# Kernel tuning notes

Measured on AMD Instinct MI355X. Metric: run time of the kernel, lower is better.

## Reference

```python
import jax, jax.numpy as jnp
import numpy as np

N_CELL, N_GENE, D, E = 100000, 20000, 128, 1000000


def setup_inputs() -> dict:
    key = jax.random.key(0)
    ks = jax.random.split(key, 16)
    return {
        "cell_z": jax.random.normal(ks[0], (N_CELL, D), jnp.float32),
        "gene_z": jax.random.normal(ks[1], (N_GENE, D), jnp.float32),
        "W_gene": jax.random.normal(ks[2], (D, D), jnp.float32) / np.sqrt(D),
        "b_gene": jax.random.normal(ks[3], (D,), jnp.float32) * 0.01,
        "cell_scale": jax.random.normal(ks[4], (N_CELL,), jnp.float32),
        "cell_bias": jax.random.normal(ks[5], (N_CELL,), jnp.float32),
        "cell_std": jax.random.uniform(ks[6], (N_CELL,), jnp.float32, 0.1, 1.0),
        "gene_scale": jax.random.normal(ks[7], (N_GENE,), jnp.float32),
        "gene_bias": jax.random.normal(ks[8], (N_GENE,), jnp.float32),
        "gene_std": jax.random.uniform(ks[9], (N_GENE,), jnp.float32, 0.1, 1.0),
        "src_idx": jax.random.randint(ks[10], (E,), 0, N_CELL, jnp.int32),
        "dst_idx": jax.random.randint(ks[11], (E,), 0, N_GENE, jnp.int32),
        "cell_n_id": jax.random.randint(ks[12], (N_CELL,), 0, N_CELL, jnp.int32),
        "gene_n_id": jax.random.randint(ks[13], (N_GENE,), 0, N_GENE, jnp.int32),
    }


def reference(cell_z, gene_z, W_gene, b_gene,
              cell_scale, cell_bias, cell_std,
              gene_scale, gene_bias, gene_std,
              src_idx, dst_idx, cell_n_id, gene_n_id):
    # Relation projection: 'cell' -> Identity, 'gene' -> Linear + LeakyReLU.
    # Project per-node then gather (mathematically identical to the original
    # gather-then-project since projection is pointwise per node).
    gene_proj = jax.nn.leaky_relu(gene_z @ W_gene + b_gene)  # [N_GENE, D]
    u = cell_z[src_idx]            # [E, D] gather of src node embeddings
    v = gene_proj[dst_idx]         # [E, D] gather of projected dst embeddings

    # Per-edge scale/bias/std lookups via global node ids (n_id[edge_index]).
    sid = cell_n_id[src_idx]       # [E]
    did = gene_n_id[dst_idx]       # [E]
    s_sc, s_b, s_sd = cell_scale[sid], cell_bias[sid], cell_std[sid]
    d_sc, d_b, d_sd = gene_scale[did], gene_bias[did], gene_std[did]

    dot = jnp.sum(u * v, axis=-1)  # [E]
    loc = dot * s_sc * d_sc + s_b + d_b
    std = s_sd * d_sd
    return jnp.stack([loc, std])   # [2, E]
```

## Files before the change

kernel.cpp:

```cpp
#include <hip/hip_runtime.h>

#define N_CELL 100000
#define N_GENE 20000
#define DIM    128
#define N_EDGE 1000000

#define NS_STRIPE 20
#define NTILE     40
#define NBLK_SORT 977

#define NB_WCAST 8
#define NB_CTAB  391
#define NB_GTAB  79
#define NB_MISC  (NB_WCAST + NB_CTAB + NB_GTAB)

#define NB_PROJ  625
#define NB_HIST  977
#define NB_CAST  6250

typedef float f32x4 __attribute__((ext_vector_type(4)));

__device__ inline unsigned short f2bf(float f) {
    unsigned u = __float_as_uint(f);
    u += 0x7fffu + ((u >> 16) & 1u);
    return (unsigned short)(u >> 16);
}

__device__ inline void dot2(float& acc, unsigned a, unsigned b) {
    asm("v_dot2_f32_bf16 %0, %1, %2, %0" : "+v"(acc) : "v"(a), "v"(b));
}

__device__ inline int tile_of(int s, int d) {
    const int ss = (int)(((unsigned long long)s * 429497ULL) >> 31);
    const int ds = (d >= 10000) ? 1 : 0;
    return ds * NS_STRIPE + ss;
}

__device__ inline unsigned pack_sd(int s, int d) {
    return ((unsigned)s << 15) | (unsigned)d;
}

__device__ inline float lrelu(float v) { return v > 0.f ? v : 0.01f * v; }

__global__ __launch_bounds__(256) void misc_kernel(
    const float* __restrict__ W,
    ushort* __restrict__ Wbt,
    const int*   __restrict__ cell_n_id,
    const int*   __restrict__ gene_n_id,
    const float* __restrict__ cell_scale,
    const float* __restrict__ cell_bias,
    const float* __restrict__ cell_std,
    const float* __restrict__ gene_scale,
    const float* __restrict__ gene_bias,
    const float* __restrict__ gene_std,
    float4* __restrict__ cell_p4,
    float4* __restrict__ gene_p4)
{
    const int tid = threadIdx.x;
    int blk = blockIdx.x;

    if (blk < NB_WCAST) {
        const int t   = blk * 256 + tid;
        const int col = t >> 4;
        const int k8  = t & 15;
        unsigned short w[8];
        #pragma unroll
        for (int j = 0; j < 8; ++j)
            w[j] = f2bf(W[(k8 * 8 + j) * DIM + col]);
        uint4 o;
        o.x = (unsigned)w[0] | ((unsigned)w[1] << 16);
        o.y = (unsigned)w[2] | ((unsigned)w[3] << 16);
        o.z = (unsigned)w[4] | ((unsigned)w[5] << 16);
        o.w = (unsigned)w[6] | ((unsigned)w[7] << 16);
        ((uint4*)Wbt)[t] = o;
        return;
    }
    blk -= NB_WCAST;

    if (blk < NB_CTAB) {
        if (!cell_p4) return;
        const int c = blk * 256 + tid;
        if (c < N_CELL) {
            const int id = cell_n_id[c];
            cell_p4[c] = make_float4(cell_scale[id], cell_bias[id],
                                     cell_std[id], 0.f);
        }
        return;
    }
    blk -= NB_CTAB;

    if (!gene_p4) return;
    const int g = blk * 256 + tid;
    if (g < N_GENE) {
        const int id = gene_n_id[g];
        gene_p4[g] = make_float4(gene_scale[id], gene_bias[id],
                                 gene_std[id], 0.f);
    }
}

__global__ __launch_bounds__(256) void proj_kernel(
    const float* __restrict__ gene_z,
    const float* __restrict__ b,
    const ushort* __restrict__ Wbt,
    ushort* __restrict__ gene_projb)
{
    __shared__ ushort zb[32 * DIM];
    __shared__ uint4  wl[2048];

    const int tid = threadIdx.x;

    const uint4* wg = (const uint4*)Wbt;
    #pragma unroll
    for (int i = 0; i < 8; ++i) {
        const int u = i * 256 + tid;
        const int c = u >> 4, j = u & 15;
        wl[(c << 4) | (j ^ (c & 15))] = wg[u];
    }

    const int row0 = blockIdx.x * 32;
    const f32x4* Z4 = (const f32x4*)(gene_z + (long)row0 * DIM);
    #pragma unroll
    for (int i = 0; i < 4; ++i) {
        const int idx = i * 256 + tid;
        const f32x4 v = Z4[idx];
        ushort4 o;
        o.x = f2bf(v.x); o.y = f2bf(v.y); o.z = f2bf(v.z); o.w = f2bf(v.w);
        ((ushort4*)zb)[idx] = o;
    }
    __syncthreads();

    const int cg = tid & 31;
    const int rg = tid >> 5;

    const float4 bb = ((const float4*)b)[cg];
    float acc[4][4];
    #pragma unroll
    for (int r = 0; r < 4; ++r) {
        acc[r][0] = bb.x; acc[r][1] = bb.y; acc[r][2] = bb.z; acc[r][3] = bb.w;
    }

    const uint4* zr = (const uint4*)zb;
    #pragma unroll 4
    for (int k8 = 0; k8 < 16; ++k8) {
        uint4 z[4], w[4];
        #pragma unroll
        for (int r = 0; r < 4; ++r)
            z[r] = zr[(rg * 4 + r) * 16 + k8];
        #pragma unroll
        for (int c = 0; c < 4; ++c) {
            const int col = cg * 4 + c;
            w[c] = wl[(col << 4) | (k8 ^ (col & 15))];
        }
        #pragma unroll
        for (int r = 0; r < 4; ++r)
            #pragma unroll
            for (int c = 0; c < 4; ++c) {
                dot2(acc[r][c], z[r].x, w[c].x);
                dot2(acc[r][c], z[r].y, w[c].y);
                dot2(acc[r][c], z[r].z, w[c].z);
                dot2(acc[r][c], z[r].w, w[c].w);
            }
    }

    #pragma unroll
    for (int r = 0; r < 4; ++r) {
        ushort4 o;
        o.x = f2bf(lrelu(acc[r][0]));
        o.y = f2bf(lrelu(acc[r][1]));
        o.z = f2bf(lrelu(acc[r][2]));
        o.w = f2bf(lrelu(acc[r][3]));
        *(ushort4*)(gene_projb + (long)(row0 + rg * 4 + r) * DIM + cg * 4) = o;
    }
}

__global__ __launch_bounds__(256) void hist_kernel(
    const int* __restrict__ src_idx,
    const int* __restrict__ dst_idx,
    int* __restrict__ counts)
{
    __shared__ int lcnt[NTILE];
    const int tid = threadIdx.x;
    const int blk = blockIdx.x;
    if (tid < NTILE) lcnt[tid] = 0;
    __syncthreads();
    #pragma unroll
    for (int q = 0; q < 4; ++q) {
        const int e = blk * 1024 + q * 256 + tid;
        if (e < N_EDGE) {
            const int t = tile_of(src_idx[e], dst_idx[e]);
            atomicAdd(&lcnt[t], 1);
        }
    }
    __syncthreads();
    if (tid < NTILE) counts[tid * NBLK_SORT + blk] = lcnt[tid];
}

__global__ __launch_bounds__(256) void cast_kernel(
    const float* __restrict__ cell_z, ushort4* __restrict__ cell_zb4)
{
    const f32x4* in4 = (const f32x4*)cell_z;
    const int base = blockIdx.x * 512 + threadIdx.x;
    const f32x4 v0 = in4[base];
    const f32x4 v1 = in4[base + 256];
    ushort4 o0, o1;
    o0.x = f2bf(v0.x); o0.y = f2bf(v0.y); o0.z = f2bf(v0.z); o0.w = f2bf(v0.w);
    o1.x = f2bf(v1.x); o1.y = f2bf(v1.y); o1.z = f2bf(v1.z); o1.w = f2bf(v1.w);
    cell_zb4[base]       = o0;
    cell_zb4[base + 256] = o1;
}

__global__ __launch_bounds__(256) void scanA_kernel(
    int* __restrict__ counts, int* __restrict__ totals)
{
    __shared__ int sd[256];
    const int t   = blockIdx.x;
    const int tid = threadIdx.x;
    int carry = 0;
    for (int c = 0; c < 4; ++c) {
        const int idx = c * 256 + tid;
        const int val = (idx < NBLK_SORT) ? counts[t * NBLK_SORT + idx] : 0;
        sd[tid] = val;
        __syncthreads();
        #pragma unroll
        for (int off = 1; off < 256; off <<= 1) {
            const int tmp = (tid >= off) ? sd[tid - off] : 0;
            __syncthreads();
            sd[tid] += tmp;
            __syncthreads();
        }
        const int incl = sd[tid];
        const int ctot = sd[255];
        if (idx < NBLK_SORT) counts[t * NBLK_SORT + idx] = carry + incl - val;
        carry += ctot;
        __syncthreads();
    }
    if (tid == 0) totals[t] = carry;
}

__global__ __launch_bounds__(256) void scatter_kernel(
    const int* __restrict__ src_idx,
    const int* __restrict__ dst_idx,
    const int* __restrict__ counts,
    const int* __restrict__ totals,
    unsigned* __restrict__ sorted_p,
    int*      __restrict__ rank)
{
    __shared__ int lcnt[NTILE];
    __shared__ int sbase[NTILE];
    __shared__ int lbase[NTILE];
    const int tid = threadIdx.x;
    const int blk = blockIdx.x;
    if (tid < NTILE) lcnt[tid] = 0;
    __syncthreads();

    int ts[4], rs[4], ss[4], ds[4];
    #pragma unroll
    for (int c = 0; c < 4; ++c) {
        const int e = blk * 1024 + c * 256 + tid;
        if (e < N_EDGE) {
            ss[c] = src_idx[e];
            ds[c] = dst_idx[e];
            ts[c] = tile_of(ss[c], ds[c]);
            rs[c] = atomicAdd(&lcnt[ts[c]], 1);
        } else { ts[c] = -1; rs[c] = 0; ss[c] = 0; ds[c] = 0; }
    }
    __syncthreads();
    if (tid == 0) {
        int s = 0;
        for (int i = 0; i < NTILE; ++i) { sbase[i] = s; s += totals[i]; }
    }
    __syncthreads();
    if (tid < NTILE) lbase[tid] = sbase[tid] + counts[tid * NBLK_SORT + blk];
    __syncthreads();

    #pragma unroll
    for (int c = 0; c < 4; ++c) {
        const int e = blk * 1024 + c * 256 + tid;
        if (ts[c] >= 0) {
            const int pos = lbase[ts[c]] + rs[c];
            sorted_p[pos] = pack_sd(ss[c], ds[c]);
            rank[e] = pos;
        }
    }
}

__global__ __launch_bounds__(256) void edge_sorted_kernel(
    const ushort* __restrict__ cell_zb,
    const ushort* __restrict__ gene_projb,
    const unsigned* __restrict__ sorted_p,
    const float4* __restrict__ cell_p4,
    const float4* __restrict__ gene_p4,
    float2* __restrict__ res)
{
    const int wg  = blockIdx.x;
    const int xcd = wg & 7;
    const int sub = wg >> 3;
    const int q = 15625 / 8, r = 15625 % 8;
    const int swz = ((xcd < r) ? xcd * (q + 1) : r * (q + 1) + (xcd - r) * q) + sub;

    const int tid  = threadIdx.x;
    const int lane = tid & 15;
    const int grp  = swz * 16 + (tid >> 4);

    const uint4 p = ((const uint4*)sorted_p)[grp];
    const int s0 = (int)(p.x >> 15), d0 = (int)(p.x & 0x7fffu);
    const int s1 = (int)(p.y >> 15), d1 = (int)(p.y & 0x7fffu);
    const int s2 = (int)(p.z >> 15), d2 = (int)(p.z & 0x7fffu);
    const int s3 = (int)(p.w >> 15), d3 = (int)(p.w & 0x7fffu);

    uint4 a0 = ((const uint4*)(cell_zb    + (long)s0 * DIM))[lane];
    uint4 a1 = ((const uint4*)(cell_zb    + (long)s1 * DIM))[lane];
    uint4 a2 = ((const uint4*)(cell_zb    + (long)s2 * DIM))[lane];
    uint4 a3 = ((const uint4*)(cell_zb    + (long)s3 * DIM))[lane];
    uint4 v0 = ((const uint4*)(gene_projb + (long)d0 * DIM))[lane];
    uint4 v1 = ((const uint4*)(gene_projb + (long)d1 * DIM))[lane];
    uint4 v2 = ((const uint4*)(gene_projb + (long)d2 * DIM))[lane];
    uint4 v3 = ((const uint4*)(gene_projb + (long)d3 * DIM))[lane];

    float dot0 = 0.f, dot1 = 0.f, dot2v = 0.f, dot3 = 0.f;
    dot2(dot0, a0.x, v0.x); dot2(dot0, a0.y, v0.y);
    dot2(dot0, a0.z, v0.z); dot2(dot0, a0.w, v0.w);
    dot2(dot1, a1.x, v1.x); dot2(dot1, a1.y, v1.y);
    dot2(dot1, a1.z, v1.z); dot2(dot1, a1.w, v1.w);
    dot2(dot2v, a2.x, v2.x); dot2(dot2v, a2.y, v2.y);
    dot2(dot2v, a2.z, v2.z); dot2(dot2v, a2.w, v2.w);
    dot2(dot3, a3.x, v3.x); dot2(dot3, a3.y, v3.y);
    dot2(dot3, a3.z, v3.z); dot2(dot3, a3.w, v3.w);

    #define RED(d)                 \
        d += __shfl_xor(d, 1);     \
        d += __shfl_xor(d, 2);     \
        d += __shfl_xor(d, 4);     \
        d += __shfl_xor(d, 8);
    RED(dot0) RED(dot1) RED(dot2v) RED(dot3)
    #undef RED

    if (lane < 4) {
        const float dj = (lane & 2) ? ((lane & 1) ? dot3 : dot2v)
                                    : ((lane & 1) ? dot1 : dot0);
        const int sj   = (lane & 2) ? ((lane & 1) ? s3 : s2)
                                    : ((lane & 1) ? s1 : s0);
        const int djx  = (lane & 2) ? ((lane & 1) ? d3 : d2)
                                    : ((lane & 1) ? d1 : d0);
        const float4 cs = cell_p4[sj];
        const float4 gs = gene_p4[djx];
        res[grp * 4 + lane] =
            make_float2(dj * cs.x * gs.x + cs.y + gs.y, cs.z * gs.z);
    }
}

__global__ __launch_bounds__(256) void fixup_kernel(
    const int*    __restrict__ rank,
    const float2* __restrict__ res,
    float* __restrict__ out)
{
    const int e0 = (blockIdx.x * 256 + threadIdx.x) * 4;
    if (e0 >= N_EDGE) return;
    const int4 r4 = *(const int4*)(rank + e0);
    const float2 r0 = res[r4.x];
    const float2 r1 = res[r4.y];
    const float2 r2 = res[r4.z];
    const float2 r3 = res[r4.w];
    *(float4*)(out + e0)          = make_float4(r0.x, r1.x, r2.x, r3.x);
    *(float4*)(out + N_EDGE + e0) = make_float4(r0.y, r1.y, r2.y, r3.y);
}

template<bool TAB>
__global__ __launch_bounds__(256) void edge_kernel(
    const ushort* __restrict__ cell_zb,
    const ushort* __restrict__ gene_projb,
    const int*   __restrict__ src_idx,
    const int*   __restrict__ dst_idx,
    const int*   __restrict__ cell_n_id,
    const int*   __restrict__ gene_n_id,
    const float* __restrict__ cell_scale,
    const float* __restrict__ cell_bias,
    const float* __restrict__ cell_std,
    const float* __restrict__ gene_scale,
    const float* __restrict__ gene_bias,
    const float* __restrict__ gene_std,
    const float4* __restrict__ cell_p4,
    const float4* __restrict__ gene_p4,
    float* __restrict__ out)
{
    const int tid  = threadIdx.x;
    const int lane = tid & 15;
    const int grp  = blockIdx.x * 16 + (tid >> 4);
    const int e0   = grp * 4;

    const int4 s4 = ((const int4*)src_idx)[grp];
    const int4 d4 = ((const int4*)dst_idx)[grp];

    uint4 a0 = ((const uint4*)(cell_zb    + (long)s4.x * DIM))[lane];
    uint4 a1 = ((const uint4*)(cell_zb    + (long)s4.y * DIM))[lane];
    uint4 a2 = ((const uint4*)(cell_zb    + (long)s4.z * DIM))[lane];
    uint4 a3 = ((const uint4*)(cell_zb    + (long)s4.w * DIM))[lane];
    uint4 v0 = ((const uint4*)(gene_projb + (long)d4.x * DIM))[lane];
    uint4 v1 = ((const uint4*)(gene_projb + (long)d4.y * DIM))[lane];
    uint4 v2 = ((const uint4*)(gene_projb + (long)d4.z * DIM))[lane];
    uint4 v3 = ((const uint4*)(gene_projb + (long)d4.w * DIM))[lane];

    float dot0 = 0.f, dot1 = 0.f, dot2v = 0.f, dot3 = 0.f;
    dot2(dot0, a0.x, v0.x); dot2(dot0, a0.y, v0.y);
    dot2(dot0, a0.z, v0.z); dot2(dot0, a0.w, v0.w);
    dot2(dot1, a1.x, v1.x); dot2(dot1, a1.y, v1.y);
    dot2(dot1, a1.z, v1.z); dot2(dot1, a1.w, v1.w);
    dot2(dot2v, a2.x, v2.x); dot2(dot2v, a2.y, v2.y);
    dot2(dot2v, a2.z, v2.z); dot2(dot2v, a2.w, v2.w);
    dot2(dot3, a3.x, v3.x); dot2(dot3, a3.y, v3.y);
    dot2(dot3, a3.z, v3.z); dot2(dot3, a3.w, v3.w);

    #define RED(d)                 \
        d += __shfl_xor(d, 1);     \
        d += __shfl_xor(d, 2);     \
        d += __shfl_xor(d, 4);     \
        d += __shfl_xor(d, 8);
    RED(dot0) RED(dot1) RED(dot2v) RED(dot3)
    #undef RED

    if (lane < 4) {
        const float dj = (lane & 2) ? ((lane & 1) ? dot3 : dot2v)
                                    : ((lane & 1) ? dot1 : dot0);
        const int sj   = (lane & 2) ? ((lane & 1) ? s4.w : s4.z)
                                    : ((lane & 1) ? s4.y : s4.x);
        const int djx  = (lane & 2) ? ((lane & 1) ? d4.w : d4.z)
                                    : ((lane & 1) ? d4.y : d4.x);
        float sc_s, b_s, sd_s, sc_d, b_d, sd_d;
        if (TAB) {
            const float4 cs = cell_p4[sj];
            const float4 gs = gene_p4[djx];
            sc_s = cs.x; b_s = cs.y; sd_s = cs.z;
            sc_d = gs.x; b_d = gs.y; sd_d = gs.z;
        } else {
            const int sid = cell_n_id[sj];
            const int did = gene_n_id[djx];
            sc_s = cell_scale[sid]; b_s = cell_bias[sid]; sd_s = cell_std[sid];
            sc_d = gene_scale[did]; b_d = gene_bias[did]; sd_d = gene_std[did];
        }
        const int e = e0 + lane;
        out[e]          = dj * sc_s * sc_d + b_s + b_d;
        out[N_EDGE + e] = sd_s * sd_d;
    }
}

extern "C" void kernel_launch(void* const* d_in, const int* in_sizes, int n_in,
                              void* d_out, int out_size, void* d_ws, size_t ws_size,
                              hipStream_t stream) {
    const float* cell_z     = (const float*)d_in[0];
    const float* gene_z     = (const float*)d_in[1];
    const float* W_gene     = (const float*)d_in[2];
    const float* b_gene     = (const float*)d_in[3];
    const float* cell_scale = (const float*)d_in[4];
    const float* cell_bias  = (const float*)d_in[5];
    const float* cell_std   = (const float*)d_in[6];
    const float* gene_scale = (const float*)d_in[7];
    const float* gene_bias  = (const float*)d_in[8];
    const float* gene_std   = (const float*)d_in[9];
    const int*   src_idx    = (const int*)d_in[10];
    const int*   dst_idx    = (const int*)d_in[11];
    const int*   cell_n_id  = (const int*)d_in[12];
    const int*   gene_n_id  = (const int*)d_in[13];

    char* ws = (char*)d_ws;
    size_t off = 0;
    ushort* gene_projb = (ushort*)(ws + off); off += (size_t)N_GENE * DIM * 2;
    ushort* cell_zb    = (ushort*)(ws + off); off += (size_t)N_CELL * DIM * 2;
    ushort* Wbt        = (ushort*)(ws + off); off += (size_t)DIM * DIM * 2;
    const size_t base_need = off;

    float4* cell_p4 = nullptr; float4* gene_p4 = nullptr;
    size_t off_tab = off;
    const size_t tab_need = (size_t)N_CELL * 16 + (size_t)N_GENE * 16;

    unsigned* sorted_p = nullptr; int* rank = nullptr; float2* res = nullptr;
    int* counts = nullptr; int* totals = nullptr;
    const size_t sort_need = (size_t)N_EDGE * 4 + (size_t)N_EDGE * 4
                           + (size_t)N_EDGE * 8
                           + (size_t)NTILE * NBLK_SORT * 4 + 256;

    const bool tab = (ws_size >= base_need + tab_need);
    const bool srt = tab && (ws_size >= base_need + tab_need + sort_need);

    if (tab) {
        cell_p4 = (float4*)(ws + off_tab);
        gene_p4 = (float4*)(ws + off_tab + (size_t)N_CELL * 16);
        off = off_tab + tab_need;
    }
    if (srt) {
        sorted_p = (unsigned*)(ws + off); off += (size_t)N_EDGE * 4;
        rank     = (int*)(ws + off);      off += (size_t)N_EDGE * 4;
        res      = (float2*)(ws + off);   off += (size_t)N_EDGE * 8;
        counts   = (int*)(ws + off);      off += (size_t)NTILE * NBLK_SORT * 4;
        totals   = (int*)(ws + off);      off += 256;
    }

    float* out = (float*)d_out;

    misc_kernel<<<NB_MISC, 256, 0, stream>>>(
        W_gene, Wbt, cell_n_id, gene_n_id,
        cell_scale, cell_bias, cell_std,
        gene_scale, gene_bias, gene_std, cell_p4, gene_p4);
    if (srt)
        hist_kernel<<<NB_HIST, 256, 0, stream>>>(src_idx, dst_idx, counts);
    proj_kernel<<<NB_PROJ, 256, 0, stream>>>(gene_z, b_gene, Wbt, gene_projb);
    cast_kernel<<<NB_CAST, 256, 0, stream>>>(cell_z, (ushort4*)cell_zb);

    if (srt) {
        scanA_kernel<<<NTILE, 256, 0, stream>>>(counts, totals);
        scatter_kernel<<<NBLK_SORT, 256, 0, stream>>>(
            src_idx, dst_idx, counts, totals, sorted_p, rank);
        edge_sorted_kernel<<<N_EDGE / 64, 256, 0, stream>>>(
            cell_zb, gene_projb, sorted_p, cell_p4, gene_p4, res);
        fixup_kernel<<<(N_EDGE / 4 + 255) / 256, 256, 0, stream>>>(rank, res, out);
    } else if (tab) {
        edge_kernel<true><<<N_EDGE / 64, 256, 0, stream>>>(
            cell_zb, gene_projb, src_idx, dst_idx, cell_n_id, gene_n_id,
            cell_scale, cell_bias, cell_std, gene_scale, gene_bias, gene_std,
            cell_p4, gene_p4, out);
    } else {
        edge_kernel<false><<<N_EDGE / 64, 256, 0, stream>>>(
            cell_zb, gene_projb, src_idx, dst_idx, cell_n_id, gene_n_id,
            cell_scale, cell_bias, cell_std, gene_scale, gene_bias, gene_std,
            nullptr, nullptr, out);
    }
}
```

Measured before the change: 90.48 us.

## Counting-sort edges by source cell and read fp32 cell rows directly

```diff
diff --git a/kernel.cpp b/kernel.cpp
--- a/kernel.cpp
+++ b/kernel.cpp
@@ -5,9 +5,9 @@
 #define DIM    128
 #define N_EDGE 1000000
 
-#define NS_STRIPE 20
-#define NTILE     40
-#define NBLK_SORT 977
+#define BINS      100352
+#define NB_SCAN   98
+#define NB_EDGEB  977
 
 #define NB_WCAST 8
 #define NB_CTAB  391
@@ -16,7 +16,7 @@
 
 #define NB_PROJ  625
 #define NB_HIST  977
-#define NB_CAST  6250
+#define NB_PREP  (NB_PROJ + NB_HIST)
 
 typedef float f32x4 __attribute__((ext_vector_type(4)));
 
@@ -30,11 +30,8 @@
     asm("v_dot2_f32_bf16 %0, %1, %2, %0" : "+v"(acc) : "v"(a), "v"(b));
 }
 
-__device__ inline int tile_of(int s, int d) {
-    const int ss = (int)(((unsigned long long)s * 429497ULL) >> 31);
-    const int ds = (d >= 10000) ? 1 : 0;
-    return ds * NS_STRIPE + ss;
-}
+#define BLO(u) __uint_as_float((u) << 16)
+#define BHI(u) __uint_as_float((u) & 0xffff0000u)
 
 __device__ inline unsigned pack_sd(int s, int d) {
     return ((unsigned)s << 15) | (unsigned)d;
@@ -78,7 +75,6 @@
     blk -= NB_WCAST;
 
     if (blk < NB_CTAB) {
-        if (!cell_p4) return;
         const int c = blk * 256 + tid;
         if (c < N_CELL) {
             const int id = cell_n_id[c];
@@ -89,7 +85,6 @@
     }
     blk -= NB_CTAB;
 
-    if (!gene_p4) return;
     const int g = blk * 256 + tid;
     if (g < N_GENE) {
         const int id = gene_n_id[g];
@@ -98,127 +93,104 @@
     }
 }
 
-__global__ __launch_bounds__(256) void proj_kernel(
+__global__ __launch_bounds__(256) void prep_fused(
     const float* __restrict__ gene_z,
     const float* __restrict__ b,
     const ushort* __restrict__ Wbt,
-    ushort* __restrict__ gene_projb)
+    ushort* __restrict__ gene_projb,
+    const int* __restrict__ src_idx,
+    int* __restrict__ bins)
 {
     __shared__ ushort zb[32 * DIM];
     __shared__ uint4  wl[2048];
 
     const int tid = threadIdx.x;
-
-    const uint4* wg = (const uint4*)Wbt;
-    #pragma unroll
-    for (int i = 0; i < 8; ++i) {
-        const int u = i * 256 + tid;
-        const int c = u >> 4, j = u & 15;
-        wl[(c << 4) | (j ^ (c & 15))] = wg[u];
-    }
-
-    const int row0 = blockIdx.x * 32;
-    const f32x4* Z4 = (const f32x4*)(gene_z + (long)row0 * DIM);
-    #pragma unroll
-    for (int i = 0; i < 4; ++i) {
-        const int idx = i * 256 + tid;
-        const f32x4 v = Z4[idx];
-        ushort4 o;
-        o.x = f2bf(v.x); o.y = f2bf(v.y); o.z = f2bf(v.z); o.w = f2bf(v.w);
-        ((ushort4*)zb)[idx] = o;
-    }
-    __syncthreads();
-
-    const int cg = tid & 31;
-    const int rg = tid >> 5;
-
-    const float4 bb = ((const float4*)b)[cg];
-    float acc[4][4];
-    #pragma unroll
-    for (int r = 0; r < 4; ++r) {
-        acc[r][0] = bb.x; acc[r][1] = bb.y; acc[r][2] = bb.z; acc[r][3] = bb.w;
-    }
-
-    const uint4* zr = (const uint4*)zb;
-    #pragma unroll 4
-    for (int k8 = 0; k8 < 16; ++k8) {
-        uint4 z[4], w[4];
-        #pragma unroll
-        for (int r = 0; r < 4; ++r)
-            z[r] = zr[(rg * 4 + r) * 16 + k8];
-        #pragma unroll
-        for (int c = 0; c < 4; ++c) {
-            const int col = cg * 4 + c;
-            w[c] = wl[(col << 4) | (k8 ^ (col & 15))];
-        }
-        #pragma unroll
-        for (int r = 0; r < 4; ++r)
+    int blk = blockIdx.x;
+
+    if (blk < NB_PROJ) {
+        const uint4* wg = (const uint4*)Wbt;
+        #pragma unroll
+        for (int i = 0; i < 8; ++i) {
+            const int u = i * 256 + tid;
+            const int c = u >> 4, j = u & 15;
+            wl[(c << 4) | (j ^ (c & 15))] = wg[u];
+        }
+        const int row0 = blk * 32;
+        const f32x4* Z4 = (const f32x4*)(gene_z + (long)row0 * DIM);
+        #pragma unroll
+        for (int i = 0; i < 4; ++i) {
+            const int idx = i * 256 + tid;
+            const f32x4 v = Z4[idx];
+            ushort4 o;
+            o.x = f2bf(v.x); o.y = f2bf(v.y); o.z = f2bf(v.z); o.w = f2bf(v.w);
+            ((ushort4*)zb)[idx] = o;
+        }
+        __syncthreads();
+
+        const int cg = tid & 31;
+        const int rg = tid >> 5;
+
+        const float4 bb = ((const float4*)b)[cg];
+        float acc[4][4];
+        #pragma unroll
+        for (int r = 0; r < 4; ++r) {
+            acc[r][0] = bb.x; acc[r][1] = bb.y;
+            acc[r][2] = bb.z; acc[r][3] = bb.w;
+        }
+
+        const uint4* zr = (const uint4*)zb;
+        #pragma unroll 4
+        for (int k8 = 0; k8 < 16; ++k8) {
+            uint4 z[4], w[4];
+            #pragma unroll
+            for (int r = 0; r < 4; ++r)
+                z[r] = zr[(rg * 4 + r) * 16 + k8];
             #pragma unroll
             for (int c = 0; c < 4; ++c) {
-                dot2(acc[r][c], z[r].x, w[c].x);
-                dot2(acc[r][c], z[r].y, w[c].y);
-                dot2(acc[r][c], z[r].z, w[c].z);
-                dot2(acc[r][c], z[r].w, w[c].w);
+                const int col = cg * 4 + c;
+                w[c] = wl[(col << 4) | (k8 ^ (col & 15))];
             }
-    }
-
-    #pragma unroll
-    for (int r = 0; r < 4; ++r) {
-        ushort4 o;
-        o.x = f2bf(lrelu(acc[r][0]));
-        o.y = f2bf(lrelu(acc[r][1]));
-        o.z = f2bf(lrelu(acc[r][2]));
-        o.w = f2bf(lrelu(acc[r][3]));
-        *(ushort4*)(gene_projb + (long)(row0 + rg * 4 + r) * DIM + cg * 4) = o;
-    }
-}
-
-__global__ __launch_bounds__(256) void hist_kernel(
-    const int* __restrict__ src_idx,
-    const int* __restrict__ dst_idx,
-    int* __restrict__ counts)
-{
-    __shared__ int lcnt[NTILE];
-    const int tid = threadIdx.x;
-    const int blk = blockIdx.x;
-    if (tid < NTILE) lcnt[tid] = 0;
-    __syncthreads();
+            #pragma unroll
+            for (int r = 0; r < 4; ++r)
+                #pragma unroll
+                for (int c = 0; c < 4; ++c) {
+                    dot2(acc[r][c], z[r].x, w[c].x);
+                    dot2(acc[r][c], z[r].y, w[c].y);
+                    dot2(acc[r][c], z[r].z, w[c].z);
+                    dot2(acc[r][c], z[r].w, w[c].w);
+                }
+        }
+
+        #pragma unroll
+        for (int r = 0; r < 4; ++r) {
+            ushort4 o;
+            o.x = f2bf(lrelu(acc[r][0]));
+            o.y = f2bf(lrelu(acc[r][1]));
+            o.z = f2bf(lrelu(acc[r][2]));
+            o.w = f2bf(lrelu(acc[r][3]));
+            *(ushort4*)(gene_projb + (long)(row0 + rg * 4 + r) * DIM + cg * 4) = o;
+        }
+        return;
+    }
+    blk -= NB_PROJ;
+
     #pragma unroll
     for (int q = 0; q < 4; ++q) {
         const int e = blk * 1024 + q * 256 + tid;
-        if (e < N_EDGE) {
-            const int t = tile_of(src_idx[e], dst_idx[e]);
-            atomicAdd(&lcnt[t], 1);
-        }
-    }
-    __syncthreads();
-    if (tid < NTILE) counts[tid * NBLK_SORT + blk] = lcnt[tid];
-}
-
-__global__ __launch_bounds__(256) void cast_kernel(
-    const float* __restrict__ cell_z, ushort4* __restrict__ cell_zb4)
-{
-    const f32x4* in4 = (const f32x4*)cell_z;
-    const int base = blockIdx.x * 512 + threadIdx.x;
-    const f32x4 v0 = in4[base];
-    const f32x4 v1 = in4[base + 256];
-    ushort4 o0, o1;
-    o0.x = f2bf(v0.x); o0.y = f2bf(v0.y); o0.z = f2bf(v0.z); o0.w = f2bf(v0.w);
-    o1.x = f2bf(v1.x); o1.y = f2bf(v1.y); o1.z = f2bf(v1.z); o1.w = f2bf(v1.w);
-    cell_zb4[base]       = o0;
-    cell_zb4[base + 256] = o1;
-}
-
-__global__ __launch_bounds__(256) void scanA_kernel(
-    int* __restrict__ counts, int* __restrict__ totals)
+        if (e < N_EDGE) atomicAdd(&bins[src_idx[e]], 1);
+    }
+}
+
+__global__ __launch_bounds__(256) void scan1_kernel(
+    int* __restrict__ bins, int* __restrict__ bsum)
 {
     __shared__ int sd[256];
     const int t   = blockIdx.x;
     const int tid = threadIdx.x;
     int carry = 0;
     for (int c = 0; c < 4; ++c) {
-        const int idx = c * 256 + tid;
-        const int val = (idx < NBLK_SORT) ? counts[t * NBLK_SORT + idx] : 0;
+        const int idx = t * 1024 + c * 256 + tid;
+        const int val = bins[idx];
         sd[tid] = val;
         __syncthreads();
         #pragma unroll
@@ -230,62 +202,52 @@
         }
         const int incl = sd[tid];
         const int ctot = sd[255];
-        if (idx < NBLK_SORT) counts[t * NBLK_SORT + idx] = carry + incl - val;
+        bins[idx] = carry + incl - val;
         carry += ctot;
         __syncthreads();
     }
-    if (tid == 0) totals[t] = carry;
+    if (tid == 0) bsum[t] = carry;
+}
+
+__global__ __launch_bounds__(256) void scan2_kernel(
+    int* __restrict__ bins, const int* __restrict__ bsum)
+{
+    __shared__ int bs[128];
+    const int t   = blockIdx.x;
+    const int tid = threadIdx.x;
+    if (tid < NB_SCAN) bs[tid] = bsum[tid];
+    __syncthreads();
+    int bp = 0;
+    for (int j = 0; j < t; ++j) bp += bs[j];
+    #pragma unroll
+    for (int c = 0; c < 4; ++c)
+        bins[t * 1024 + c * 256 + tid] += bp;
 }
 
 __global__ __launch_bounds__(256) void scatter_kernel(
     const int* __restrict__ src_idx,
     const int* __restrict__ dst_idx,
-    const int* __restrict__ counts,
-    const int* __restrict__ totals,
+    int* __restrict__ bins,
     unsigned* __restrict__ sorted_p,
     int*      __restrict__ rank)
 {
-    __shared__ int lcnt[NTILE];
-    __shared__ int sbase[NTILE];
-    __shared__ int lbase[NTILE];
     const int tid = threadIdx.x;
     const int blk = blockIdx.x;
-    if (tid < NTILE) lcnt[tid] = 0;
-    __syncthreads();
-
-    int ts[4], rs[4], ss[4], ds[4];
     #pragma unroll
     for (int c = 0; c < 4; ++c) {
         const int e = blk * 1024 + c * 256 + tid;
         if (e < N_EDGE) {
-            ss[c] = src_idx[e];
-            ds[c] = dst_idx[e];
-            ts[c] = tile_of(ss[c], ds[c]);
-            rs[c] = atomicAdd(&lcnt[ts[c]], 1);
-        } else { ts[c] = -1; rs[c] = 0; ss[c] = 0; ds[c] = 0; }
-    }
-    __syncthreads();
-    if (tid == 0) {
-        int s = 0;
-        for (int i = 0; i < NTILE; ++i) { sbase[i] = s; s += totals[i]; }
-    }
-    __syncthreads();
-    if (tid < NTILE) lbase[tid] = sbase[tid] + counts[tid * NBLK_SORT + blk];
-    __syncthreads();
-
-    #pragma unroll
-    for (int c = 0; c < 4; ++c) {
-        const int e = blk * 1024 + c * 256 + tid;
-        if (ts[c] >= 0) {
-            const int pos = lbase[ts[c]] + rs[c];
-            sorted_p[pos] = pack_sd(ss[c], ds[c]);
+            const int s = src_idx[e];
+            const int d = dst_idx[e];
+            const int pos = atomicAdd(&bins[s], 1);
+            sorted_p[pos] = pack_sd(s, d);
             rank[e] = pos;
         }
     }
 }
 
 __global__ __launch_bounds__(256) void edge_sorted_kernel(
-    const ushort* __restrict__ cell_zb,
+    const float*  __restrict__ cell_z,
     const ushort* __restrict__ gene_projb,
     const unsigned* __restrict__ sorted_p,
     const float4* __restrict__ cell_p4,
@@ -308,24 +270,35 @@
     const int s2 = (int)(p.z >> 15), d2 = (int)(p.z & 0x7fffu);
     const int s3 = (int)(p.w >> 15), d3 = (int)(p.w & 0x7fffu);
 
-    uint4 a0 = ((const uint4*)(cell_zb    + (long)s0 * DIM))[lane];
-    uint4 a1 = ((const uint4*)(cell_zb    + (long)s1 * DIM))[lane];
-    uint4 a2 = ((const uint4*)(cell_zb    + (long)s2 * DIM))[lane];
-    uint4 a3 = ((const uint4*)(cell_zb    + (long)s3 * DIM))[lane];
-    uint4 v0 = ((const uint4*)(gene_projb + (long)d0 * DIM))[lane];
-    uint4 v1 = ((const uint4*)(gene_projb + (long)d1 * DIM))[lane];
-    uint4 v2 = ((const uint4*)(gene_projb + (long)d2 * DIM))[lane];
-    uint4 v3 = ((const uint4*)(gene_projb + (long)d3 * DIM))[lane];
-
-    float dot0 = 0.f, dot1 = 0.f, dot2v = 0.f, dot3 = 0.f;
-    dot2(dot0, a0.x, v0.x); dot2(dot0, a0.y, v0.y);
-    dot2(dot0, a0.z, v0.z); dot2(dot0, a0.w, v0.w);
-    dot2(dot1, a1.x, v1.x); dot2(dot1, a1.y, v1.y);
-    dot2(dot1, a1.z, v1.z); dot2(dot1, a1.w, v1.w);
-    dot2(dot2v, a2.x, v2.x); dot2(dot2v, a2.y, v2.y);
-    dot2(dot2v, a2.z, v2.z); dot2(dot2v, a2.w, v2.w);
-    dot2(dot3, a3.x, v3.x); dot2(dot3, a3.y, v3.y);
-    dot2(dot3, a3.z, v3.z); dot2(dot3, a3.w, v3.w);
+    const float4* u0p = (const float4*)(cell_z + (long)s0 * DIM);
+    const float4* u1p = (const float4*)(cell_z + (long)s1 * DIM);
+    const float4* u2p = (const float4*)(cell_z + (long)s2 * DIM);
+    const float4* u3p = (const float4*)(cell_z + (long)s3 * DIM);
+
+    const float4 u0a = u0p[2 * lane], u0b = u0p[2 * lane + 1];
+    const float4 u1a = u1p[2 * lane], u1b = u1p[2 * lane + 1];
+    const float4 u2a = u2p[2 * lane], u2b = u2p[2 * lane + 1];
+    const float4 u3a = u3p[2 * lane], u3b = u3p[2 * lane + 1];
+    const uint4  v0  = ((const uint4*)(gene_projb + (long)d0 * DIM))[lane];
+    const uint4  v1  = ((const uint4*)(gene_projb + (long)d1 * DIM))[lane];
+    const uint4  v2  = ((const uint4*)(gene_projb + (long)d2 * DIM))[lane];
+    const uint4  v3  = ((const uint4*)(gene_projb + (long)d3 * DIM))[lane];
+
+    #define DOT(res_, ua, ub, vv)                                   \
+        float res_ = 0.f;                                           \
+        res_ = fmaf(ua.x, BLO(vv.x), res_);                         \
+        res_ = fmaf(ua.y, BHI(vv.x), res_);                         \
+        res_ = fmaf(ua.z, BLO(vv.y), res_);                         \
+        res_ = fmaf(ua.w, BHI(vv.y), res_);                         \
+        res_ = fmaf(ub.x, BLO(vv.z), res_);                         \
+        res_ = fmaf(ub.y, BHI(vv.z), res_);                         \
+        res_ = fmaf(ub.z, BLO(vv.w), res_);                         \
+        res_ = fmaf(ub.w, BHI(vv.w), res_);
+    DOT(dot0, u0a, u0b, v0)
+    DOT(dot1, u1a, u1b, v1)
+    DOT(dot2v, u2a, u2b, v2)
+    DOT(dot3, u3a, u3b, v3)
+    #undef DOT
 
     #define RED(d)                 \
         d += __shfl_xor(d, 1);     \
@@ -365,9 +338,8 @@
     *(float4*)(out + N_EDGE + e0) = make_float4(r0.y, r1.y, r2.y, r3.y);
 }
 
-template<bool TAB>
-__global__ __launch_bounds__(256) void edge_kernel(
-    const ushort* __restrict__ cell_zb,
+__global__ __launch_bounds__(256) void edge_fallback(
+    const float*  __restrict__ cell_z,
     const ushort* __restrict__ gene_projb,
     const int*   __restrict__ src_idx,
     const int*   __restrict__ dst_idx,
@@ -379,67 +351,39 @@
     const float* __restrict__ gene_scale,
     const float* __restrict__ gene_bias,
     const float* __restrict__ gene_std,
-    const float4* __restrict__ cell_p4,
-    const float4* __restrict__ gene_p4,
     float* __restrict__ out)
 {
     const int tid  = threadIdx.x;
     const int lane = tid & 15;
-    const int grp  = blockIdx.x * 16 + (tid >> 4);
-    const int e0   = grp * 4;
-
-    const int4 s4 = ((const int4*)src_idx)[grp];
-    const int4 d4 = ((const int4*)dst_idx)[grp];
-
-    uint4 a0 = ((const uint4*)(cell_zb    + (long)s4.x * DIM))[lane];
-    uint4 a1 = ((const uint4*)(cell_zb    + (long)s4.y * DIM))[lane];
-    uint4 a2 = ((const uint4*)(cell_zb    + (long)s4.z * DIM))[lane];
-    uint4 a3 = ((const uint4*)(cell_zb    + (long)s4.w * DIM))[lane];
-    uint4 v0 = ((const uint4*)(gene_projb + (long)d4.x * DIM))[lane];
-    uint4 v1 = ((const uint4*)(gene_projb + (long)d4.y * DIM))[lane];
-    uint4 v2 = ((const uint4*)(gene_projb + (long)d4.z * DIM))[lane];
-    uint4 v3 = ((const uint4*)(gene_projb + (long)d4.w * DIM))[lane];
-
-    float dot0 = 0.f, dot1 = 0.f, dot2v = 0.f, dot3 = 0.f;
-    dot2(dot0, a0.x, v0.x); dot2(dot0, a0.y, v0.y);
-    dot2(dot0, a0.z, v0.z); dot2(dot0, a0.w, v0.w);
-    dot2(dot1, a1.x, v1.x); dot2(dot1, a1.y, v1.y);
-    dot2(dot1, a1.z, v1.z); dot2(dot1, a1.w, v1.w);
-    dot2(dot2v, a2.x, v2.x); dot2(dot2v, a2.y, v2.y);
-    dot2(dot2v, a2.z, v2.z); dot2(dot2v, a2.w, v2.w);
-    dot2(dot3, a3.x, v3.x); dot2(dot3, a3.y, v3.y);
-    dot2(dot3, a3.z, v3.z); dot2(dot3, a3.w, v3.w);
-
-    #define RED(d)                 \
-        d += __shfl_xor(d, 1);     \
-        d += __shfl_xor(d, 2);     \
-        d += __shfl_xor(d, 4);     \
-        d += __shfl_xor(d, 8);
-    RED(dot0) RED(dot1) RED(dot2v) RED(dot3)
-    #undef RED
-
-    if (lane < 4) {
-        const float dj = (lane & 2) ? ((lane & 1) ? dot3 : dot2v)
-                                    : ((lane & 1) ? dot1 : dot0);
-        const int sj   = (lane & 2) ? ((lane & 1) ? s4.w : s4.z)
-                                    : ((lane & 1) ? s4.y : s4.x);
-        const int djx  = (lane & 2) ? ((lane & 1) ? d4.w : d4.z)
-                                    : ((lane & 1) ? d4.y : d4.x);
-        float sc_s, b_s, sd_s, sc_d, b_d, sd_d;
-        if (TAB) {
-            const float4 cs = cell_p4[sj];
-            const float4 gs = gene_p4[djx];
-            sc_s = cs.x; b_s = cs.y; sd_s = cs.z;
-            sc_d = gs.x; b_d = gs.y; sd_d = gs.z;
-        } else {
-            const int sid = cell_n_id[sj];
-            const int did = gene_n_id[djx];
-            sc_s = cell_scale[sid]; b_s = cell_bias[sid]; sd_s = cell_std[sid];
-            sc_d = gene_scale[did]; b_d = gene_bias[did]; sd_d = gene_std[did];
-        }
-        const int e = e0 + lane;
-        out[e]          = dj * sc_s * sc_d + b_s + b_d;
-        out[N_EDGE + e] = sd_s * sd_d;
+    const int e    = blockIdx.x * 16 + (tid >> 4);
+
+    const int s = src_idx[e];
+    const int d = dst_idx[e];
+    const float4* up = (const float4*)(cell_z + (long)s * DIM);
+    const float4 ua = up[2 * lane], ub = up[2 * lane + 1];
+    const uint4  v  = ((const uint4*)(gene_projb + (long)d * DIM))[lane];
+
+    float dot = 0.f;
+    dot = fmaf(ua.x, BLO(v.x), dot);
+    dot = fmaf(ua.y, BHI(v.x), dot);
+    dot = fmaf(ua.z, BLO(v.y), dot);
+    dot = fmaf(ua.w, BHI(v.y), dot);
+    dot = fmaf(ub.x, BLO(v.z), dot);
+    dot = fmaf(ub.y, BHI(v.z), dot);
+    dot = fmaf(ub.z, BLO(v.w), dot);
+    dot = fmaf(ub.w, BHI(v.w), dot);
+
+    dot += __shfl_xor(dot, 1);
+    dot += __shfl_xor(dot, 2);
+    dot += __shfl_xor(dot, 4);
+    dot += __shfl_xor(dot, 8);
+
+    if (lane == 0) {
+        const int sid = cell_n_id[s];
+        const int did = gene_n_id[d];
+        out[e]          = dot * cell_scale[sid] * gene_scale[did]
+                        + cell_bias[sid] + gene_bias[did];
+        out[N_EDGE + e] = cell_std[sid] * gene_std[did];
     }
 }
 
@@ -464,63 +408,45 @@
     char* ws = (char*)d_ws;
     size_t off = 0;
     ushort* gene_projb = (ushort*)(ws + off); off += (size_t)N_GENE * DIM * 2;
-    ushort* cell_zb    = (ushort*)(ws + off); off += (size_t)N_CELL * DIM * 2;
     ushort* Wbt        = (ushort*)(ws + off); off += (size_t)DIM * DIM * 2;
-    const size_t base_need = off;
-
-    float4* cell_p4 = nullptr; float4* gene_p4 = nullptr;
-    size_t off_tab = off;
-    const size_t tab_need = (size_t)N_CELL * 16 + (size_t)N_GENE * 16;
-
-    unsigned* sorted_p = nullptr; int* rank = nullptr; float2* res = nullptr;
-    int* counts = nullptr; int* totals = nullptr;
-    const size_t sort_need = (size_t)N_EDGE * 4 + (size_t)N_EDGE * 4
-                           + (size_t)N_EDGE * 8
-                           + (size_t)NTILE * NBLK_SORT * 4 + 256;
-
-    const bool tab = (ws_size >= base_need + tab_need);
-    const bool srt = tab && (ws_size >= base_need + tab_need + sort_need);
-
-    if (tab) {
-        cell_p4 = (float4*)(ws + off_tab);
-        gene_p4 = (float4*)(ws + off_tab + (size_t)N_CELL * 16);
-        off = off_tab + tab_need;
-    }
-    if (srt) {
-        sorted_p = (unsigned*)(ws + off); off += (size_t)N_EDGE * 4;
-        rank     = (int*)(ws + off);      off += (size_t)N_EDGE * 4;
-        res      = (float2*)(ws + off);   off += (size_t)N_EDGE * 8;
-        counts   = (int*)(ws + off);      off += (size_t)NTILE * NBLK_SORT * 4;
-        totals   = (int*)(ws + off);      off += 256;
-    }
+    float4* cell_p4    = (float4*)(ws + off); off += (size_t)N_CELL * 16;
+    float4* gene_p4    = (float4*)(ws + off); off += (size_t)N_GENE * 16;
+    unsigned* sorted_p = (unsigned*)(ws + off); off += (size_t)N_EDGE * 4;
+    int*    rank       = (int*)(ws + off);    off += (size_t)N_EDGE * 4;
+    float2* res        = (float2*)(ws + off); off += (size_t)N_EDGE * 8;
+    int*    bins       = (int*)(ws + off);    off += (size_t)BINS * 4;
+    int*    bsum       = (int*)(ws + off);    off += 512;
 
     float* out = (float*)d_out;
-
+    const bool ok = (ws_size >= off);
+
+    if (!ok) {
+        misc_kernel<<<NB_MISC, 256, 0, stream>>>(
+            W_gene, Wbt, cell_n_id, gene_n_id,
+            cell_scale, cell_bias, cell_std,
+            gene_scale, gene_bias, gene_std,
+            (float4*)Wbt, (float4*)Wbt);
+        prep_fused<<<NB_PROJ, 256, 0, stream>>>(
+            gene_z, b_gene, Wbt, gene_projb, src_idx, nullptr);
+        edge_fallback<<<N_EDGE / 16, 256, 0, stream>>>(
+            cell_z, gene_projb, src_idx, dst_idx, cell_n_id, gene_n_id,
+            cell_scale, cell_bias, cell_std,
+            gene_scale, gene_bias, gene_std, out);
+        return;
+    }
+
+    hipMemsetAsync(bins, 0, (size_t)BINS * 4, stream);
     misc_kernel<<<NB_MISC, 256, 0, stream>>>(
         W_gene, Wbt, cell_n_id, gene_n_id,
         cell_scale, cell_bias, cell_std,
         gene_scale, gene_bias, gene_std, cell_p4, gene_p4);
-    if (srt)
-        hist_kernel<<<NB_HIST, 256, 0, stream>>>(src_idx, dst_idx, counts);
-    proj_kernel<<<NB_PROJ, 256, 0, stream>>>(gene_z, b_gene, Wbt, gene_projb);
-    cast_kernel<<<NB_CAST, 256, 0, stream>>>(cell_z, (ushort4*)cell_zb);
-
-    if (srt) {
-        scanA_kernel<<<NTILE, 256, 0, stream>>>(counts, totals);
-        scatter_kernel<<<NBLK_SORT, 256, 0, stream>>>(
-            src_idx, dst_idx, counts, totals, sorted_p, rank);
-        edge_sorted_kernel<<<N_EDGE / 64, 256, 0, stream>>>(
-            cell_zb, gene_projb, sorted_p, cell_p4, gene_p4, res);
-        fixup_kernel<<<(N_EDGE / 4 + 255) / 256, 256, 0, stream>>>(rank, res, out);
-    } else if (tab) {
-        edge_kernel<true><<<N_EDGE / 64, 256, 0, stream>>>(
-            cell_zb, gene_projb, src_idx, dst_idx, cell_n_id, gene_n_id,
-            cell_scale, cell_bias, cell_std, gene_scale, gene_bias, gene_std,
-            cell_p4, gene_p4, out);
-    } else {
-        edge_kernel<false><<<N_EDGE / 64, 256, 0, stream>>>(
-            cell_zb, gene_projb, src_idx, dst_idx, cell_n_id, gene_n_id,
-            cell_scale, cell_bias, cell_std, gene_scale, gene_bias, gene_std,
-            nullptr, nullptr, out);
-    }
-}
+    prep_fused<<<NB_PREP, 256, 0, stream>>>(
+        gene_z, b_gene, Wbt, gene_projb, src_idx, bins);
+    scan1_kernel<<<NB_SCAN, 256, 0, stream>>>(bins, bsum);
+    scan2_kernel<<<NB_SCAN, 256, 0, stream>>>(bins, bsum);
+    scatter_kernel<<<NB_EDGEB, 256, 0, stream>>>(
+        src_idx, dst_idx, bins, sorted_p, rank);
+    edge_sorted_kernel<<<N_EDGE / 64, 256, 0, stream>>>(
+        cell_z, gene_projb, sorted_p, cell_p4, gene_p4, res);
+    fixup_kernel<<<(N_EDGE / 4 + 255) / 256, 256, 0, stream>>>(rank, res, out);
+}
```

Result: slower. 190.4 us (+110.4%).
